# Kernel optimization log

Hardware: AMD Instinct MI355X
Metric: run time of the kernel (lower is better)

Reference implementation:

```python
import jax, jax.numpy as jnp
import numpy as np

B, S, D_MODEL = 2, 2048, 2048
D_STATE, D_CONV, EXPAND = 16, 4, 2
D_INNER = EXPAND * D_MODEL  # 4096


def setup_inputs() -> dict:
    key = jax.random.key(0)
    ks = jax.random.split(key, 7)
    nrm = lambda k, shape, sc: jax.random.normal(k, shape, jnp.float32) * sc
    x = nrm(ks[0], (B, S, D_MODEL), 1.0)
    W_in = nrm(ks[1], (2 * D_INNER, D_MODEL), 0.02)          # in_proj (no bias)
    conv_w = nrm(ks[2], (D_INNER, 1, D_CONV), 0.1)            # depthwise conv1d
    conv_b = nrm(ks[3], (D_INNER,), 0.02)
    W_dt = nrm(ks[4], (D_INNER, D_INNER), 0.001)              # dt_proj weight
    b_dt = jnp.full((D_INNER,), -8.0, jnp.float32)            # keeps softplus(dt) tiny -> stable scan
    A_log = jnp.log(jnp.arange(1, D_STATE + 1, dtype=jnp.float32))[None, :]  # [1, d_state]
    W_out = nrm(ks[5], (D_MODEL, D_INNER), 1e-4)              # out_proj (no bias)
    return dict(x=x, W_in=W_in, conv_w=conv_w, conv_b=conv_b,
                W_dt=W_dt, b_dt=b_dt, A_log=A_log, W_out=W_out)


def reference(x, W_in, conv_w, conv_b, W_dt, b_dt, A_log, W_out):
    # in_proj then split into ssm branch and gate
    xz = jnp.einsum('bsd,ed->bse', x, W_in)            # [B,S,2*D_INNER]
    xi, gate = jnp.split(xz, 2, axis=-1)
    # depthwise causal conv (torch pads d_conv-1 both sides then truncates to S == left-pad only)
    xc = jnp.transpose(xi, (0, 2, 1))                  # [B,D_INNER,S]
    xc = jax.lax.conv_general_dilated(
        xc, conv_w, window_strides=(1,), padding=[(D_CONV - 1, 0)],
        dimension_numbers=('NCH', 'OIH', 'NCH'), feature_group_count=D_INNER)
    xc = xc + conv_b[None, :, None]
    xs = jax.nn.silu(jnp.transpose(xc, (0, 2, 1)))     # [B,S,D_INNER]
    # selective scan (only first d_state channels of x and dt are used)
    A = -jnp.exp(A_log[0])                             # [D_STATE]
    dt = jax.nn.softplus(jnp.einsum('bsd,ed->bse', xs, W_dt[:D_STATE]) + b_dt[:D_STATE])  # [B,S,D_STATE]
    u = xs[:, :, :D_STATE]                             # [B,S,D_STATE]

    def step(h, inp):
        x_t, dt_t = inp
        h = h * (1.0 + dt_t) + x_t
        return h, (h * A).sum(-1)                      # y_t: [B]

    h0 = jnp.zeros((B, D_STATE), xs.dtype)
    _, ys = jax.lax.scan(step, h0, (jnp.swapaxes(u, 0, 1), jnp.swapaxes(dt, 0, 1)))
    result = jnp.swapaxes(ys, 0, 1)                    # [B,S]
    # original: expand to d_inner, sum (== *d_inner), broadcast back over d_inner
    ssm_out = jnp.broadcast_to((result * D_INNER)[..., None], (B, S, D_INNER))
    y = ssm_out * jax.nn.sigmoid(gate)
    return jnp.einsum('bse,de->bsd', y, W_out)         # [B,S,D_MODEL]
```

## Files before the change

### kernel.cpp

```cpp
#include <hip/hip_runtime.h>
#include <hip/hip_bf16.h>
#include <math.h>

using bf16_t = __bf16;
using bf16x4 = __attribute__((ext_vector_type(4))) __bf16;
using bf16x8 = __attribute__((ext_vector_type(8))) __bf16;
using f32x4  = __attribute__((ext_vector_type(4))) float;

typedef __attribute__((address_space(1))) const void* gas_ptr;
typedef __attribute__((address_space(3))) void*       las_ptr;

#define BATCH    2
#define SEQ      2048
#define DMODEL   2048
#define DINNER   4096
#define DSTATE   16
#define NROWS    (BATCH * SEQ)

#define CAST_C0  (2 * DINNER * DMODEL / 8)
#define CAST_C1  (NROWS * DMODEL / 8)
#define CAST_C2  (DMODEL * DINNER / 8)
#define CAST_C3  (DSTATE * DINNER / 8)
#define CAST_BLOCKS ((CAST_C0 + CAST_C1 + CAST_C2 + CAST_C3) / 256)

__global__ __launch_bounds__(256)
void cast_all_kernel(const float* __restrict__ s0, bf16_t* __restrict__ d0,
                     const float* __restrict__ s1, bf16_t* __restrict__ d1,
                     const float* __restrict__ s2, bf16_t* __restrict__ d2,
                     const float* __restrict__ s3, bf16_t* __restrict__ d3)
{
    int i = blockIdx.x * 256 + threadIdx.x;
    const float* src; bf16_t* dst; int j;
    if (i < CAST_C0)                            { src = s0; dst = d0; j = i; }
    else if (i < CAST_C0 + CAST_C1)             { src = s1; dst = d1; j = i - CAST_C0; }
    else if (i < CAST_C0 + CAST_C1 + CAST_C2)   { src = s2; dst = d2; j = i - CAST_C0 - CAST_C1; }
    else                                        { src = s3; dst = d3; j = i - CAST_C0 - CAST_C1 - CAST_C2; }
    size_t off = (size_t)j * 8;
    float4 a = *(const float4*)(src + off);
    float4 b = *(const float4*)(src + off + 4);
    bf16x8 o;
    o[0] = (bf16_t)a.x; o[1] = (bf16_t)a.y; o[2] = (bf16_t)a.z; o[3] = (bf16_t)a.w;
    o[4] = (bf16_t)b.x; o[5] = (bf16_t)b.y; o[6] = (bf16_t)b.z; o[7] = (bf16_t)b.w;
    *(bf16x8*)(dst + off) = o;
}

#define GBAR()     asm volatile("s_barrier" ::: "memory")
#define WLGKM0()   asm volatile("s_waitcnt lgkmcnt(0)" ::: "memory")
#define WVM0()     asm volatile("s_waitcnt vmcnt(0)" ::: "memory")

#define MM(m, n, av, bv) \
    acc[m][n] = __builtin_amdgcn_mfma_f32_16x16x32_bf16(av, bv, acc[m][n], 0, 0, 0)

#define MFMA_COL2(nA, nB, bA, bB)                                   \
    MM(0, nA, a0, bA); MM(0, nB, a0, bB); MM(1, nA, a1, bA); MM(1, nB, a1, bB); \
    MM(2, nA, a2, bA); MM(2, nB, a2, bB); MM(3, nA, a3, bA); MM(3, nB, a3, bB); \
    MM(4, nA, a4, bA); MM(4, nB, a4, bB); MM(5, nA, a5, bA); MM(5, nB, a5, bB); \
    MM(6, nA, a6, bA); MM(6, nB, a6, bB); MM(7, nA, a7, bA); MM(7, nB, a7, bB)

__global__ __launch_bounds__(512, 2)
void gemm1_256(const bf16_t* __restrict__ A, const bf16_t* __restrict__ B,
               float* __restrict__ outf, bf16_t* __restrict__ outg)
{
    constexpr int K  = DMODEL;
    constexpr int NT = K / 64;

    __shared__ bf16_t As[2][256 * 64];
    __shared__ bf16_t Bs[2][256 * 64];

    const int t    = threadIdx.x;
    const int w    = t >> 6;
    const int lane = t & 63;
    const int wm   = w >> 2;
    const int wn   = w & 3;
    const int lo   = lane & 15;
    const int q    = lane >> 4;
    const int swz  = lo & 7;

    const int m0 = blockIdx.y * 256;
    const int n0 = blockIdx.x * 256;

    const int r_l   = lane >> 3;
    const int cb    = (lane & 7) ^ r_l;
    const int laneg = r_l * K + cb * 8;

    const bf16_t* Abase = A + (size_t)(m0 + w * 32) * K;
    const bf16_t* Bbase = B + (size_t)(n0 + w * 32) * K;

#define STAGE_A(BUF, kk) do {                                                  \
    _Pragma("unroll")                                                          \
    for (int c = 0; c < 4; ++c)                                                \
        __builtin_amdgcn_global_load_lds(                                      \
            (gas_ptr)(Abase + (kk) + c * 8 * K + laneg),                       \
            (las_ptr)&As[BUF][(w * 32 + c * 8) * 64], 16, 0, 0);               \
} while (0)
#define STAGE_B(BUF, kk) do {                                                  \
    _Pragma("unroll")                                                          \
    for (int c = 0; c < 4; ++c)                                                \
        __builtin_amdgcn_global_load_lds(                                      \
            (gas_ptr)(Bbase + (kk) + c * 8 * K + laneg),                       \
            (las_ptr)&Bs[BUF][(w * 32 + c * 8) * 64], 16, 0, 0);               \
} while (0)

#define LDA_F(BUF, m, s) \
    (*(const bf16x8*)&As[BUF][(wm * 128 + (m) * 16 + lo) * 64 + ((((s) * 4 + q) ^ swz) * 8)])
#define LDB_F(BUF, n, s) \
    (*(const bf16x8*)&Bs[BUF][(wn * 64  + (n) * 16 + lo) * 64 + ((((s) * 4 + q) ^ swz) * 8)])

    f32x4 acc[8][4];
#pragma unroll
    for (int i = 0; i < 8; ++i)
#pragma unroll
        for (int j = 0; j < 4; ++j) acc[i][j] = (f32x4){0.f, 0.f, 0.f, 0.f};

    STAGE_A(0, 0);
    STAGE_B(0, 0);
    WVM0();
    GBAR();

#define TILE_STEP(CUR, NXT, tkv) do {                                          \
    const int  k1_  = ((tkv) + 1) * 64;                                        \
    const bool pre_ = ((tkv) + 1) < NT;                                        \
    bf16x8 a0, a1, a2, a3, a4, a5, a6, a7, b0, b1, b2, b3;                     \
                   \
    a0 = LDA_F(CUR, 0, 0); a1 = LDA_F(CUR, 1, 0);                              \
    a2 = LDA_F(CUR, 2, 0); a3 = LDA_F(CUR, 3, 0);                              \
    a4 = LDA_F(CUR, 4, 0); a5 = LDA_F(CUR, 5, 0);                              \
    a6 = LDA_F(CUR, 6, 0); a7 = LDA_F(CUR, 7, 0);                              \
    b0 = LDB_F(CUR, 0, 0); b1 = LDB_F(CUR, 1, 0);                              \
    if (pre_) STAGE_A(NXT, k1_);                                               \
    GBAR(); WLGKM0();                                                          \
    __builtin_amdgcn_s_setprio(1);                                             \
    MFMA_COL2(0, 1, b0, b1);                                                   \
    __builtin_amdgcn_s_setprio(0);                                             \
    GBAR();                                                                    \
                                \
    b2 = LDB_F(CUR, 2, 0); b3 = LDB_F(CUR, 3, 0);                              \
    if (pre_) STAGE_B(NXT, k1_);                                               \
    GBAR(); WLGKM0();                                                          \
    __builtin_amdgcn_s_setprio(1);                                             \
    MFMA_COL2(2, 3, b2, b3);                                                   \
    __builtin_amdgcn_s_setprio(0);                                             \
    GBAR();                                                                    \
                                  \
    a0 = LDA_F(CUR, 0, 1); a1 = LDA_F(CUR, 1, 1);                              \
    a2 = LDA_F(CUR, 2, 1); a3 = LDA_F(CUR, 3, 1);                              \
    a4 = LDA_F(CUR, 4, 1); a5 = LDA_F(CUR, 5, 1);                              \
    a6 = LDA_F(CUR, 6, 1); a7 = LDA_F(CUR, 7, 1);                              \
    b0 = LDB_F(CUR, 0, 1); b1 = LDB_F(CUR, 1, 1);                              \
    GBAR(); WLGKM0();                                                          \
    __builtin_amdgcn_s_setprio(1);                                             \
    MFMA_COL2(0, 1, b0, b1);                                                   \
    __builtin_amdgcn_s_setprio(0);                                             \
    GBAR();                                                                    \
           \
    b2 = LDB_F(CUR, 2, 1); b3 = LDB_F(CUR, 3, 1);                              \
    GBAR(); WLGKM0();                                                          \
    __builtin_amdgcn_s_setprio(1);                                             \
    MFMA_COL2(2, 3, b2, b3);                                                   \
    __builtin_amdgcn_s_setprio(0);                                             \
    WVM0();                                                                    \
    GBAR();                                                                    \
} while (0)

#pragma unroll 1
    for (int tk = 0; tk < NT; tk += 2) {
        TILE_STEP(0, 1, tk);
        TILE_STEP(1, 0, tk + 1);
    }

#pragma unroll
    for (int m = 0; m < 8; ++m) {
        const int rbase = m0 + wm * 128 + m * 16 + q * 4;
#pragma unroll
        for (int n = 0; n < 4; ++n) {
            const int col = n0 + wn * 64 + n * 16 + lo;
#pragma unroll
            for (int rr = 0; rr < 4; ++rr) {
                float v   = acc[m][n][rr];
                int   row = rbase + rr;
                if (col < DINNER) {
                    outf[(size_t)row * DINNER + col] = v;
                } else {
                    float sg = 1.f / (1.f + __expf(-v));
                    outg[(size_t)row * DINNER + (col - DINNER)] = (bf16_t)sg;
                }
            }
        }
    }
}

__global__ __launch_bounds__(256)
void gemm_bt2(const bf16_t* __restrict__ A, const bf16_t* __restrict__ B, int K,
              float* __restrict__ outf, const float* __restrict__ rowscale)
{
    constexpr int LDK = 64;
    __shared__ bf16_t As[128 * LDK];
    __shared__ bf16_t Bs[128 * LDK];

    const int t    = threadIdx.x;
    const int m0   = blockIdx.y * 128;
    const int n0   = blockIdx.x * 128;
    const int w    = t >> 6;
    const int lane = t & 63;
    const int wr   = (w >> 1) * 64;
    const int wc   = (w & 1) * 64;
    const int lo   = lane & 15;
    const int q    = lane >> 4;

    const int r_l  = lane >> 3;
    const int cb   = (lane & 7) ^ r_l;
    const int laneA = (w * 32 + r_l) * K + cb * 8;
    const bf16_t* Abase = A + (size_t)m0 * K;
    const bf16_t* Bbase = B + (size_t)n0 * K;

    f32x4 acc[4][4];
#pragma unroll
    for (int i = 0; i < 4; ++i)
#pragma unroll
        for (int j = 0; j < 4; ++j) acc[i][j] = (f32x4){0.f, 0.f, 0.f, 0.f};

    for (int k0 = 0; k0 < K; k0 += 64) {
#pragma unroll
        for (int c = 0; c < 4; ++c) {
            const int uoff   = k0 + c * 8 * K;
            const int lo_off = (w * 32 + c * 8) * LDK;
            __builtin_amdgcn_global_load_lds((gas_ptr)(Abase + uoff + laneA),
                                             (las_ptr)&As[lo_off], 16, 0, 0);
            __builtin_amdgcn_global_load_lds((gas_ptr)(Bbase + uoff + laneA),
                                             (las_ptr)&Bs[lo_off], 16, 0, 0);
        }
        __syncthreads();

        const int swz = lo & 7;
#pragma unroll
        for (int ks = 0; ks < 2; ++ks) {
            const int kk = ((ks * 4 + q) ^ swz) * 8;
            bf16x8 af[4], bfv[4];
#pragma unroll
            for (int mi = 0; mi < 4; ++mi)
                af[mi] = *(const bf16x8*)&As[(wr + mi * 16 + lo) * LDK + kk];
#pragma unroll
            for (int ni = 0; ni < 4; ++ni)
                bfv[ni] = *(const bf16x8*)&Bs[(wc + ni * 16 + lo) * LDK + kk];
#pragma unroll
            for (int mi = 0; mi < 4; ++mi)
#pragma unroll
                for (int ni = 0; ni < 4; ++ni)
                    acc[mi][ni] = __builtin_amdgcn_mfma_f32_16x16x32_bf16(
                        af[mi], bfv[ni], acc[mi][ni], 0, 0, 0);
        }
        __syncthreads();
    }

#pragma unroll
    for (int mi = 0; mi < 4; ++mi) {
#pragma unroll
        for (int ni = 0; ni < 4; ++ni) {
            const int col   = n0 + wc + ni * 16 + lo;
            const int rbase = m0 + wr + mi * 16 + q * 4;
#pragma unroll
            for (int rr = 0; rr < 4; ++rr) {
                int row = rbase + rr;
                outf[(size_t)row * DMODEL + col] =
                    acc[mi][ni][rr] * (4096.0f * rowscale[row]);
            }
        }
    }
}

#define RROWS 4
__global__ __launch_bounds__(256)
void conv_silu_kernel(const float* __restrict__ xi, const float* __restrict__ cw,
                      const float* __restrict__ cbias,
                      bf16_t* __restrict__ xs, float* __restrict__ uT)
{
    const int r0 = blockIdx.x * RROWS;
    const int t  = threadIdx.x;
    const int s0 = r0 & (SEQ - 1);
    const int b  = r0 >> 11;

#pragma unroll
    for (int j = 0; j < 4; ++j) {
        const int c = t * 4 + j * 1024;
        float4 w0 = *(const float4*)(cw + (c + 0) * 4);
        float4 w1 = *(const float4*)(cw + (c + 1) * 4);
        float4 w2 = *(const float4*)(cw + (c + 2) * 4);
        float4 w3 = *(const float4*)(cw + (c + 3) * 4);
        float4 cbv = *(const float4*)(cbias + c);
        float4 xr[RROWS + 3];
#pragma unroll
        for (int i = 0; i < RROWS + 3; ++i) {
            int ss = s0 - 3 + i;
            if (ss >= 0)
                xr[i] = *(const float4*)(xi + (size_t)(r0 - 3 + i) * DINNER + c);
            else
                xr[i] = make_float4(0.f, 0.f, 0.f, 0.f);
        }
#pragma unroll
        for (int rr = 0; rr < RROWS; ++rr) {
            float4 a = xr[rr], bv = xr[rr + 1], cc = xr[rr + 2], d = xr[rr + 3];
            float v0 = cbv.x + w0.x * a.x + w0.y * bv.x + w0.z * cc.x + w0.w * d.x;
            float v1 = cbv.y + w1.x * a.y + w1.y * bv.y + w1.z * cc.y + w1.w * d.y;
            float v2 = cbv.z + w2.x * a.z + w2.y * bv.z + w2.z * cc.z + w2.w * d.z;
            float v3 = cbv.w + w3.x * a.w + w3.y * bv.w + w3.z * cc.w + w3.w * d.w;
            float o0 = v0 / (1.f + __expf(-v0));
            float o1 = v1 / (1.f + __expf(-v1));
            float o2 = v2 / (1.f + __expf(-v2));
            float o3 = v3 / (1.f + __expf(-v3));
            bf16x4 ov;
            ov[0] = (bf16_t)o0; ov[1] = (bf16_t)o1;
            ov[2] = (bf16_t)o2; ov[3] = (bf16_t)o3;
            *(bf16x4*)(xs + (size_t)(r0 + rr) * DINNER + c) = ov;
            if (j == 0 && t < 4) {
                uT[b * (DSTATE * SEQ) + (c + 0) * SEQ + (s0 + rr)] = o0;
                uT[b * (DSTATE * SEQ) + (c + 1) * SEQ + (s0 + rr)] = o1;
                uT[b * (DSTATE * SEQ) + (c + 2) * SEQ + (s0 + rr)] = o2;
                uT[b * (DSTATE * SEQ) + (c + 3) * SEQ + (s0 + rr)] = o3;
            }
        }
    }
}

__global__ __launch_bounds__(256)
void dt_mfma_kernel(const bf16_t* __restrict__ xs, const bf16_t* __restrict__ wdtb,
                    const float* __restrict__ bdt, float* __restrict__ dtT)
{
    __shared__ float red[4][256];
    const int t    = threadIdx.x;
    const int w    = t >> 6;
    const int lane = t & 63;
    const int lo   = lane & 15;
    const int q    = lane >> 4;
    const int r0   = blockIdx.x * 16;

    const bf16_t* arow = xs   + (size_t)(r0 + lo) * DINNER + w * 1024 + q * 8;
    const bf16_t* brow = wdtb + (size_t)lo        * DINNER + w * 1024 + q * 8;

    f32x4 acc = (f32x4){0.f, 0.f, 0.f, 0.f};
#pragma unroll
    for (int kt = 0; kt < 32; ++kt) {
        bf16x8 a  = *(const bf16x8*)(arow + kt * 32);
        bf16x8 bv = *(const bf16x8*)(brow + kt * 32);
        acc = __builtin_amdgcn_mfma_f32_16x16x32_bf16(a, bv, acc, 0, 0, 0);
    }
#pragma unroll
    for (int i = 0; i < 4; ++i) red[w][lane * 4 + i] = acc[i];
    __syncthreads();

    {
        const int ln  = t >> 2;
        const int i   = t & 3;
        const int e   = ln & 15;
        const int row = r0 + (ln >> 4) * 4 + i;
        float v = red[0][t] + red[1][t] + red[2][t] + red[3][t] + bdt[e];
        float dtv = (v > 20.f) ? v : log1pf(__expf(v));
        dtT[(row >> 11) * (DSTATE * SEQ) + e * SEQ + (row & (SEQ - 1))] = dtv;
    }
}

__global__ __launch_bounds__(512)
void scan2_kernel(const float* __restrict__ dtT, const float* __restrict__ uT,
                  const float* __restrict__ A_log, float* __restrict__ result)
{
    __shared__ float cont[SEQ * 17];
    __shared__ float segP[DSTATE][32];
    __shared__ float segH[DSTATE][32];
    __shared__ float hin[DSTATE][32];

    const int b   = blockIdx.x;
    const int t   = threadIdx.x;
    const int n   = t >> 5;
    const int seg = t & 31;
    const float An = -expf(A_log[n]);

    const float* dtp = dtT + b * (DSTATE * SEQ) + n * SEQ + seg * 64;
    const float* up  = uT  + b * (DSTATE * SEQ) + n * SEQ + seg * 64;

    float P = 1.f, H = 0.f;
    for (int i = 0; i < 64; i += 4) {
        float4 dv = *(const float4*)(dtp + i);
        float4 uv = *(const float4*)(up + i);
        float a;
        a = 1.f + dv.x; P *= a; H = H * a + uv.x;
        a = 1.f + dv.y; P *= a; H = H * a + uv.y;
        a = 1.f + dv.z; P *= a; H = H * a + uv.z;
        a = 1.f + dv.w; P *= a; H = H * a + uv.w;
    }
    segP[n][seg] = P;
    segH[n][seg] = H;
    __syncthreads();

    if (t < DSTATE) {
        float h = 0.f;
#pragma unroll
        for (int j = 0; j < 32; ++j) {
            hin[t][j] = h;
            h = segP[t][j] * h + segH[t][j];
        }
    }
    __syncthreads();

    {
        float h = hin[n][seg];
        const int nsw = (n + seg) & 15;
        for (int i = 0; i < 64; i += 4) {
            float4 dv = *(const float4*)(dtp + i);
            float4 uv = *(const float4*)(up + i);
            const int s = seg * 64 + i;
            h = h * (1.f + dv.x) + uv.x; cont[(s + 0) * 17 + nsw] = h * An;
            h = h * (1.f + dv.y) + uv.y; cont[(s + 1) * 17 + nsw] = h * An;
            h = h * (1.f + dv.z) + uv.z; cont[(s + 2) * 17 + nsw] = h * An;
            h = h * (1.f + dv.w) + uv.w; cont[(s + 3) * 17 + nsw] = h * An;
        }
    }
    __syncthreads();

#pragma unroll
    for (int k = 0; k < 4; ++k) {
        const int s = t + k * 512;
        float sum = 0.f;
#pragma unroll
        for (int j = 0; j < DSTATE; ++j) sum += cont[s * 17 + j];
        result[b * SEQ + s] = sum;
    }
}

extern "C" void kernel_launch(void* const* d_in, const int* in_sizes, int n_in,
                              void* d_out, int out_size, void* d_ws, size_t ws_size,
                              hipStream_t stream)
{
    const float* x      = (const float*)d_in[0];
    const float* W_in   = (const float*)d_in[1];
    const float* conv_w = (const float*)d_in[2];
    const float* conv_b = (const float*)d_in[3];
    const float* W_dt   = (const float*)d_in[4];
    const float* b_dt   = (const float*)d_in[5];
    const float* A_log  = (const float*)d_in[6];
    const float* W_out  = (const float*)d_in[7];
    float* out = (float*)d_out;

    const size_t MB = 1u << 20;
    char* w = (char*)d_ws;
    bf16_t* xb   = (bf16_t*)(w);
    bf16_t* wib  = (bf16_t*)(w + 16 * MB);
    bf16_t* wob  = (bf16_t*)(w + 48 * MB);
    float*  xi   = (float*) (w + 64 * MB);
    bf16_t* g    = (bf16_t*)(w + 128 * MB);
    float*  uT   = (float*) (w + 160 * MB);
    float*  dtT  = (float*) (w + 160 * MB + 262144);
    float*  res  = (float*) (w + 160 * MB + 2 * 262144);
    bf16_t* xs   = (bf16_t*)(w + 161 * MB);
    bf16_t* wdtb = (bf16_t*)(w + 193 * MB);

    cast_all_kernel<<<CAST_BLOCKS, 256, 0, stream>>>(W_in, wib, x, xb, W_out, wob,
                                                     W_dt, wdtb);

    gemm1_256<<<dim3(32, 16), 512, 0, stream>>>(xb, wib, xi, g);

    conv_silu_kernel<<<NROWS / RROWS, 256, 0, stream>>>(xi, conv_w, conv_b, xs, uT);

    dt_mfma_kernel<<<NROWS / 16, 256, 0, stream>>>(xs, wdtb, b_dt, dtT);

    scan2_kernel<<<2, 512, 0, stream>>>(dtT, uT, A_log, res);

    gemm_bt2<<<dim3(16, 32), 256, 0, stream>>>(g, wob, DINNER, out, res);
}
```

Baseline: 465.8 us.

## Double-buffer LDS in output GEMM to overlap global loads with MFMA

Rewrites the output projection GEMM to use two LDS buffers, issuing the next K-tile's global-to-LDS loads while MFMAs run on the current tile. It also raises wave priority around the MFMA bursts and specializes K at compile time. The aim is to hide global memory latency, which the single-buffer version exposed through its two barriers per K step. In exchange, LDS use doubles, which may reduce occupancy. The code also depends on macros (MM, WVM0, GBAR, WLGKM0) that are presumably defined earlier in the file.

```diff
diff --git a/kernel.cpp b/kernel.cpp
--- a/kernel.cpp
+++ b/kernel.cpp
@@ -189,29 +189,60 @@
     }
 }
 
+#define MFMA_G16()                                                  \
+    MM(0, 0, a0, b0); MM(0, 1, a0, b1); MM(1, 0, a1, b0); MM(1, 1, a1, b1); \
+    MM(2, 0, a2, b0); MM(2, 1, a2, b1); MM(3, 0, a3, b0); MM(3, 1, a3, b1); \
+    MM(0, 2, a0, b2); MM(0, 3, a0, b3); MM(1, 2, a1, b2); MM(1, 3, a1, b3); \
+    MM(2, 2, a2, b2); MM(2, 3, a2, b3); MM(3, 2, a3, b2); MM(3, 3, a3, b3)
+
 __global__ __launch_bounds__(256)
-void gemm_bt2(const bf16_t* __restrict__ A, const bf16_t* __restrict__ B, int K,
+void gemm2_db(const bf16_t* __restrict__ A, const bf16_t* __restrict__ B,
               float* __restrict__ outf, const float* __restrict__ rowscale)
 {
-    constexpr int LDK = 64;
-    __shared__ bf16_t As[128 * LDK];
-    __shared__ bf16_t Bs[128 * LDK];
+    constexpr int K  = DINNER;
+    constexpr int NT = K / 64;
+
+    __shared__ bf16_t As2[2][128 * 64];
+    __shared__ bf16_t Bs2[2][128 * 64];
 
     const int t    = threadIdx.x;
-    const int m0   = blockIdx.y * 128;
-    const int n0   = blockIdx.x * 128;
     const int w    = t >> 6;
     const int lane = t & 63;
     const int wr   = (w >> 1) * 64;
     const int wc   = (w & 1) * 64;
     const int lo   = lane & 15;
     const int q    = lane >> 4;
-
-    const int r_l  = lane >> 3;
-    const int cb   = (lane & 7) ^ r_l;
-    const int laneA = (w * 32 + r_l) * K + cb * 8;
-    const bf16_t* Abase = A + (size_t)m0 * K;
-    const bf16_t* Bbase = B + (size_t)n0 * K;
+    const int swz  = lo & 7;
+
+    const int m0 = blockIdx.y * 128;
+    const int n0 = blockIdx.x * 128;
+
+    const int r_l   = lane >> 3;
+    const int cb    = (lane & 7) ^ r_l;
+    const int laneg = r_l * K + cb * 8;
+
+    const bf16_t* Abase = A + (size_t)(m0 + w * 32) * K;
+    const bf16_t* Bbase = B + (size_t)(n0 + w * 32) * K;
+
+#define ST2A(BUF, kk) do {                                                     \
+    _Pragma("unroll")                                                          \
+    for (int c = 0; c < 4; ++c)                                                \
+        __builtin_amdgcn_global_load_lds(                                      \
+            (gas_ptr)(Abase + (kk) + c * 8 * K + laneg),                       \
+            (las_ptr)&As2[BUF][(w * 32 + c * 8) * 64], 16, 0, 0);              \
+} while (0)
+#define ST2B(BUF, kk) do {                                                     \
+    _Pragma("unroll")                                                          \
+    for (int c = 0; c < 4; ++c)                                                \
+        __builtin_amdgcn_global_load_lds(                                      \
+            (gas_ptr)(Bbase + (kk) + c * 8 * K + laneg),                       \
+            (las_ptr)&Bs2[BUF][(w * 32 + c * 8) * 64], 16, 0, 0);              \
+} while (0)
+
+#define LD2A(BUF, m, s) \
+    (*(const bf16x8*)&As2[BUF][(wr + (m) * 16 + lo) * 64 + ((((s) * 4 + q) ^ swz) * 8)])
+#define LD2B(BUF, n, s) \
+    (*(const bf16x8*)&Bs2[BUF][(wc + (n) * 16 + lo) * 64 + ((((s) * 4 + q) ^ swz) * 8)])
 
     f32x4 acc[4][4];
 #pragma unroll
@@ -219,37 +250,43 @@
 #pragma unroll
         for (int j = 0; j < 4; ++j) acc[i][j] = (f32x4){0.f, 0.f, 0.f, 0.f};
 
-    for (int k0 = 0; k0 < K; k0 += 64) {
-#pragma unroll
-        for (int c = 0; c < 4; ++c) {
-            const int uoff   = k0 + c * 8 * K;
-            const int lo_off = (w * 32 + c * 8) * LDK;
-            __builtin_amdgcn_global_load_lds((gas_ptr)(Abase + uoff + laneA),
-                                             (las_ptr)&As[lo_off], 16, 0, 0);
-            __builtin_amdgcn_global_load_lds((gas_ptr)(Bbase + uoff + laneA),
-                                             (las_ptr)&Bs[lo_off], 16, 0, 0);
-        }
-        __syncthreads();
-
-        const int swz = lo & 7;
-#pragma unroll
-        for (int ks = 0; ks < 2; ++ks) {
-            const int kk = ((ks * 4 + q) ^ swz) * 8;
-            bf16x8 af[4], bfv[4];
-#pragma unroll
-            for (int mi = 0; mi < 4; ++mi)
-                af[mi] = *(const bf16x8*)&As[(wr + mi * 16 + lo) * LDK + kk];
-#pragma unroll
-            for (int ni = 0; ni < 4; ++ni)
-                bfv[ni] = *(const bf16x8*)&Bs[(wc + ni * 16 + lo) * LDK + kk];
-#pragma unroll
-            for (int mi = 0; mi < 4; ++mi)
-#pragma unroll
-                for (int ni = 0; ni < 4; ++ni)
-                    acc[mi][ni] = __builtin_amdgcn_mfma_f32_16x16x32_bf16(
-                        af[mi], bfv[ni], acc[mi][ni], 0, 0, 0);
-        }
-        __syncthreads();
+    ST2A(0, 0);
+    ST2B(0, 0);
+    WVM0();
+    GBAR();
+
+#define G2STEP(CUR, NXT, tkv) do {                                             \
+    const int  k1_  = ((tkv) + 1) * 64;                                        \
+    const bool pre_ = ((tkv) + 1) < NT;                                        \
+    bf16x8 a0, a1, a2, a3, b0, b1, b2, b3;                                     \
+           \
+    a0 = LD2A(CUR, 0, 0); a1 = LD2A(CUR, 1, 0);                                \
+    a2 = LD2A(CUR, 2, 0); a3 = LD2A(CUR, 3, 0);                                \
+    b0 = LD2B(CUR, 0, 0); b1 = LD2B(CUR, 1, 0);                                \
+    b2 = LD2B(CUR, 2, 0); b3 = LD2B(CUR, 3, 0);                                \
+    if (pre_) { ST2A(NXT, k1_); ST2B(NXT, k1_); }                              \
+    GBAR(); WLGKM0();                                                          \
+    __builtin_amdgcn_s_setprio(1);                                             \
+    MFMA_G16();                                                                \
+    __builtin_amdgcn_s_setprio(0);                                             \
+    GBAR();                                                                    \
+                    \
+    a0 = LD2A(CUR, 0, 1); a1 = LD2A(CUR, 1, 1);                                \
+    a2 = LD2A(CUR, 2, 1); a3 = LD2A(CUR, 3, 1);                                \
+    b0 = LD2B(CUR, 0, 1); b1 = LD2B(CUR, 1, 1);                                \
+    b2 = LD2B(CUR, 2, 1); b3 = LD2B(CUR, 3, 1);                                \
+    GBAR(); WLGKM0();                                                          \
+    __builtin_amdgcn_s_setprio(1);                                             \
+    MFMA_G16();                                                                \
+    __builtin_amdgcn_s_setprio(0);                                             \
+    WVM0();                                                                    \
+    GBAR();                                                                    \
+} while (0)
+
+#pragma unroll 1
+    for (int tk = 0; tk < NT; tk += 2) {
+        G2STEP(0, 1, tk);
+        G2STEP(1, 0, tk + 1);
     }
 
 #pragma unroll
@@ -463,5 +500,5 @@
 
     scan2_kernel<<<2, 512, 0, stream>>>(dtT, uT, A_log, res);
 
-    gemm_bt2<<<dim3(16, 32), 256, 0, stream>>>(g, wob, DINNER, out, res);
-}
+    gemm2_db<<<dim3(16, 32), 256, 0, stream>>>(g, wob, out, res);
+}
```

Result: faster. 453.8 us (-2.6%).
